# Performance work log

Hardware: AMD Instinct MI355X
Metric: run time of the kernel (lower is better)

## Reference

```python
import jax, jax.numpy as jnp
import numpy as np

N_NODES = 50000
N_EDGES = 800000
D_IN = 128
D_HID = 128
N_CLASSES = 10
N_GRAPHS = 64


def setup_inputs() -> dict:
    key = jax.random.key(0)
    ks = jax.random.split(key, 12)
    x = jax.random.normal(ks[0], (N_NODES, D_IN), dtype=jnp.float32)
    edge_index = jax.random.randint(ks[1], (2, N_EDGES), 0, N_NODES, dtype=jnp.int32)
    batch = jnp.sort(jax.random.randint(ks[2], (N_NODES,), 0, N_GRAPHS, dtype=jnp.int32))
    s = 0.05
    conv0_w = jax.random.normal(ks[3], (D_IN, D_HID), dtype=jnp.float32) * s
    conv0_b = jax.random.normal(ks[4], (D_HID,), dtype=jnp.float32) * s
    conv1_w = jax.random.normal(ks[5], (D_HID, D_HID), dtype=jnp.float32) * s
    conv1_b = jax.random.normal(ks[6], (D_HID,), dtype=jnp.float32) * s
    lin0_w = jax.random.normal(ks[7], (D_HID, D_HID), dtype=jnp.float32) * s
    lin0_b = jax.random.normal(ks[8], (D_HID,), dtype=jnp.float32) * s
    lin1_w = jax.random.normal(ks[9], (D_HID, N_CLASSES), dtype=jnp.float32) * s
    lin1_b = jax.random.normal(ks[10], (N_CLASSES,), dtype=jnp.float32) * s
    return dict(x=x, edge_index=edge_index, batch=batch,
                conv0_w=conv0_w, conv0_b=conv0_b,
                conv1_w=conv1_w, conv1_b=conv1_b,
                lin0_w=lin0_w, lin0_b=lin0_b,
                lin1_w=lin1_w, lin1_b=lin1_b)


def gcn_conv(x, edge_index, w, b):
    # PyG GCNConv: linear transform, add self-loops, D^-1/2 (A+I) D^-1/2 aggregation, + bias
    n = x.shape[0]
    h = x @ w  # [N, out]
    loop = jnp.arange(n, dtype=edge_index.dtype)
    row = jnp.concatenate([edge_index[0], loop])  # source nodes
    col = jnp.concatenate([edge_index[1], loop])  # destination nodes
    deg = jax.ops.segment_sum(jnp.ones_like(col, dtype=h.dtype), col, num_segments=n)
    dinv = jnp.where(deg > 0, jax.lax.rsqrt(deg), 0.0)
    norm = dinv[row] * dinv[col]  # [E+N]
    msg = h[row] * norm[:, None]  # gather + scale
    out = jax.ops.segment_sum(msg, col, num_segments=n)  # scatter-add
    return out + b


def reference(x, edge_index, batch, conv0_w, conv0_b, conv1_w, conv1_b,
              lin0_w, lin0_b, lin1_w, lin1_b):
    h = jax.nn.relu(gcn_conv(x, edge_index, conv0_w, conv0_b))
    h = jax.nn.relu(gcn_conv(h, edge_index, conv1_w, conv1_b))
    # global max pooling over nodes of each graph
    h = jax.ops.segment_max(h, batch, num_segments=N_GRAPHS)  # [G, D_HID]
    # NOTE: original applies relu after EVERY linear, including the output layer
    h = jax.nn.relu(h @ lin0_w + lin0_b)
    h = jax.nn.relu(h @ lin1_w + lin1_b)
    return jax.nn.log_softmax(h, axis=-1)
```

## Files before the change

kernel.cpp:

```cpp
#include <hip/hip_runtime.h>

#define D 128
#define BINCAP 6144
#define P2CAP 6144

typedef __attribute__((ext_vector_type(8))) short short8;
typedef __attribute__((ext_vector_type(4))) float f32x4;

__device__ inline unsigned short f2bf(float f) {
    unsigned u = __float_as_uint(f);
    return (unsigned short)((u + 0x7FFFu + ((u >> 16) & 1u)) >> 16);
}
__device__ inline float bflo(unsigned u) { return __uint_as_float(u << 16); }
__device__ inline float bfhi(unsigned u) { return __uint_as_float(u & 0xFFFF0000u); }

__global__ __launch_bounds__(256) void k_initW(const float* __restrict__ w0, const float* __restrict__ w1,
                                               const float* __restrict__ b0, const float* __restrict__ b1,
                                               uint4* __restrict__ Wp0, uint4* __restrict__ Wp1,
                                               float* __restrict__ b0p, float* __restrict__ b1p,
                                               int* __restrict__ binCur, int* __restrict__ pool, int nbins) {
    int t = threadIdx.x, b = blockIdx.x;
    int e = b * 256 + t;
    {
        int l = e & 63, U = (e >> 6) & 7, T = e >> 9;
        int nn = U * 16 + (l & 15);
        int kq = T * 32 + ((l >> 4) << 3);
        unsigned r[4], s[4];
#pragma unroll
        for (int jj = 0; jj < 4; ++jj) {
            int k0 = kq + 2 * jj, k1 = k0 + 1;
            unsigned a0 = f2bf(w0[k0 * 128 + nn]), a1 = f2bf(w0[k1 * 128 + nn]);
            r[jj] = a0 | (a1 << 16);
            int c0 = ((k0 & 7) << 4) | (k0 >> 3), c1 = ((k1 & 7) << 4) | (k1 >> 3);
            unsigned q0 = f2bf(w1[c0 * 128 + nn]), q1 = f2bf(w1[c1 * 128 + nn]);
            s[jj] = q0 | (q1 << 16);
        }
        Wp0[e] = make_uint4(r[0], r[1], r[2], r[3]);
        Wp1[e] = make_uint4(s[0], s[1], s[2], s[3]);
    }
    if (b == 0) {
        if (t < nbins) binCur[t] = t * BINCAP;
        for (int i = t; i < 64 * 128; i += 256) pool[i] = 0;
    }
    if (b == 1 && t < 128) {
        int c = ((t & 7) << 4) | (t >> 3);
        b0p[t] = b0[c];
        b1p[t] = b1[c];
    }
}

__global__ __launch_bounds__(256) void k_p1scatter(const int* __restrict__ row, const int* __restrict__ col,
                                                   int* __restrict__ binCur, unsigned* __restrict__ ebuf, int E) {
    __shared__ int h[256], s[256], delta[256], lcur[256];
    __shared__ unsigned stage[4096];
    int t = threadIdx.x;
    h[t] = 0;
    __syncthreads();
    int base = blockIdx.x * 4096;
    int cnt = min(4096, E - base);
    if (cnt == 4096) {
        int myc[16], myr[16];
        const int4* c4 = (const int4*)(col + base);
        const int4* r4 = (const int4*)(row + base);
#pragma unroll
        for (int k = 0; k < 4; ++k) {
            int4 cv = c4[t * 4 + k];
            int4 rv = r4[t * 4 + k];
            myc[k * 4 + 0] = cv.x; myc[k * 4 + 1] = cv.y; myc[k * 4 + 2] = cv.z; myc[k * 4 + 3] = cv.w;
            myr[k * 4 + 0] = rv.x; myr[k * 4 + 1] = rv.y; myr[k * 4 + 2] = rv.z; myr[k * 4 + 3] = rv.w;
        }
#pragma unroll
        for (int k = 0; k < 16; ++k) atomicAdd(&h[myc[k] >> 8], 1);
        __syncthreads();
        int v = h[t];
        s[t] = v;
        __syncthreads();
        for (int off = 1; off < 256; off <<= 1) {
            int tmp = (t >= off) ? s[t - off] : 0;
            __syncthreads();
            s[t] += tmp;
            __syncthreads();
        }
        int excl = s[t] - v;
        lcur[t] = excl;
        delta[t] = (v > 0) ? (atomicAdd(&binCur[t], v) - excl) : 0;
        __syncthreads();
#pragma unroll
        for (int k = 0; k < 16; ++k) {
            int d = myc[k];
            int slot = atomicAdd(&lcur[d >> 8], 1);
            stage[slot] = ((unsigned)d << 16) | (unsigned)myr[k];
        }
        __syncthreads();
#pragma unroll
        for (int k = 0; k < 16; ++k) {
            int slot = k * 256 + t;
            unsigned vv = stage[slot];
            int b = vv >> 24;
            ebuf[delta[b] + slot] = vv;
        }
    } else {
        for (int k = 0; k < 16; ++k) {
            int e = base + k * 256 + t;
            if (e < E) atomicAdd(&h[col[e] >> 8], 1);
        }
        __syncthreads();
        int v = h[t];
        s[t] = v;
        __syncthreads();
        for (int off = 1; off < 256; off <<= 1) {
            int tmp = (t >= off) ? s[t - off] : 0;
            __syncthreads();
            s[t] += tmp;
            __syncthreads();
        }
        int excl = s[t] - v;
        lcur[t] = excl;
        delta[t] = (v > 0) ? (atomicAdd(&binCur[t], v) - excl) : 0;
        __syncthreads();
        for (int k = 0; k < 16; ++k) {
            int e = base + k * 256 + t;
            if (e < E) {
                int d = col[e];
                int slot = atomicAdd(&lcur[d >> 8], 1);
                stage[slot] = ((unsigned)d << 16) | (unsigned)row[e];
            }
        }
        __syncthreads();
        for (int k = 0; k < 16; ++k) {
            int slot = k * 256 + t;
            if (slot < cnt) {
                unsigned vv = stage[slot];
                int b = vv >> 24;
                ebuf[delta[b] + slot] = vv;
            }
        }
    }
}

__global__ __launch_bounds__(256) void k_p2sort(const unsigned* __restrict__ ebuf, const int* __restrict__ binCur,
                                                int* __restrict__ csr, int* __restrict__ off_, int* __restrict__ end_,
                                                float* __restrict__ dinv, int n) {
    __shared__ unsigned stage[P2CAP];
    __shared__ unsigned stage2[P2CAP];
    __shared__ int h[256], s[256], cur[256];
    int b = blockIdx.x, t = threadIdx.x;
    int beg = b * BINCAP;
    int cnt = binCur[b] - beg;
    h[t] = 0;
    __syncthreads();
    int nfull = cnt >> 2;
    const uint4* e4 = (const uint4*)(ebuf + beg);
    uint4* st4 = (uint4*)stage;
    for (int i = t; i < nfull; i += 256) {
        uint4 v = e4[i];
        st4[i] = v;
        atomicAdd(&h[(v.x >> 16) & 0xFF], 1);
        atomicAdd(&h[(v.y >> 16) & 0xFF], 1);
        atomicAdd(&h[(v.z >> 16) & 0xFF], 1);
        atomicAdd(&h[(v.w >> 16) & 0xFF], 1);
    }
    for (int i = (nfull << 2) + t; i < cnt; i += 256) {
        unsigned v = ebuf[beg + i];
        stage[i] = v;
        atomicAdd(&h[(v >> 16) & 0xFF], 1);
    }
    __syncthreads();
    int v = h[t];
    s[t] = v;
    __syncthreads();
    for (int off = 1; off < 256; off <<= 1) {
        int tmp = (t >= off) ? s[t - off] : 0;
        __syncthreads();
        s[t] += tmp;
        __syncthreads();
    }
    int excl = s[t] - v;
    cur[t] = excl;
    int d = b * 256 + t;
    if (d < n) {
        off_[d] = beg + excl;
        end_[d] = beg + excl + v;
        dinv[d] = rsqrtf((float)(v + 1));
    }
    __syncthreads();
    for (int i = t; i < cnt; i += 256) {
        unsigned vv = stage[i];
        int slot = atomicAdd(&cur[(vv >> 16) & 0xFF], 1);
        stage2[slot] = vv & 0xFFFFu;
    }
    __syncthreads();
    uint4* c4o = (uint4*)(csr + beg);
    uint4* st24 = (uint4*)stage2;
    for (int i = t; i < nfull; i += 256) c4o[i] = st24[i];
    for (int i = (nfull << 2) + t; i < cnt; i += 256) csr[beg + i] = (int)stage2[i];
}

__global__ __launch_bounds__(256) void k_gemm0(const float* __restrict__ x, const uint4* __restrict__ Wp,
                                               const float* __restrict__ dinv, unsigned* __restrict__ outb, int n) {
    int wave = threadIdx.x >> 6, l = threadIdx.x & 63;
    int mt = blockIdx.x * 4 + wave;
    int r0 = mt * 16;
    if (r0 >= n) return;
    int rowA = r0 + (l & 15);
    int kq = (l >> 4) * 8;
    f32x4 acc[8];
#pragma unroll
    for (int U = 0; U < 8; ++U) acc[U] = (f32x4){0.f, 0.f, 0.f, 0.f};
    const float* xr = x + (size_t)rowA * 128 + kq;
#pragma unroll
    for (int T = 0; T < 4; ++T) {
        float4 a0 = *(const float4*)(xr + T * 32);
        float4 a1 = *(const float4*)(xr + T * 32 + 4);
        short8 af;
        af[0] = (short)f2bf(a0.x); af[1] = (short)f2bf(a0.y);
        af[2] = (short)f2bf(a0.z); af[3] = (short)f2bf(a0.w);
        af[4] = (short)f2bf(a1.x); af[5] = (short)f2bf(a1.y);
        af[6] = (short)f2bf(a1.z); af[7] = (short)f2bf(a1.w);
#pragma unroll
        for (int U = 0; U < 8; ++U) {
            short8 bf = *(const short8*)&Wp[(T * 8 + U) * 64 + l];
            acc[U] = __builtin_amdgcn_mfma_f32_16x16x32_bf16(af, bf, acc[U], 0, 0, 0);
        }
    }
    int rq = l >> 4, cl = l & 15;
#pragma unroll
    for (int q = 0; q < 4; ++q) {
        int rr = r0 + rq * 4 + q;
        float d = dinv[rr];
        uint4 w;
        w.x = (unsigned)f2bf(acc[0][q] * d) | ((unsigned)f2bf(acc[1][q] * d) << 16);
        w.y = (unsigned)f2bf(acc[2][q] * d) | ((unsigned)f2bf(acc[3][q] * d) << 16);
        w.z = (unsigned)f2bf(acc[4][q] * d) | ((unsigned)f2bf(acc[5][q] * d) << 16);
        w.w = (unsigned)f2bf(acc[6][q] * d) | ((unsigned)f2bf(acc[7][q] * d) << 16);
        *(uint4*)(outb + (size_t)rr * 64 + cl * 4) = w;
    }
}

__device__ inline void gather4(const uint4* __restrict__ hp4, const int* __restrict__ csr,
                               int q, int beg, int len, float acc[8]) {
    int maxlen = len;
    maxlen = max(maxlen, __shfl_xor(maxlen, 16, 64));
    maxlen = max(maxlen, __shfl_xor(maxlen, 32, 64));
    int j = 0;
    for (; j + 2 <= maxlen; j += 2) {
        bool a0 = (j < len), a1 = (j + 1 < len);
        int s0 = 0, s1 = 0;
        if (a0) s0 = csr[beg + j];
        if (a1) s1 = csr[beg + j + 1];
        uint4 u0, u1;
        if (a0) u0 = hp4[(size_t)s0 * 16 + q];
        if (a1) u1 = hp4[(size_t)s1 * 16 + q];
        if (a0) {
            acc[0] += bflo(u0.x); acc[1] += bfhi(u0.x);
            acc[2] += bflo(u0.y); acc[3] += bfhi(u0.y);
            acc[4] += bflo(u0.z); acc[5] += bfhi(u0.z);
            acc[6] += bflo(u0.w); acc[7] += bfhi(u0.w);
        }
        if (a1) {
            acc[0] += bflo(u1.x); acc[1] += bfhi(u1.x);
            acc[2] += bflo(u1.y); acc[3] += bfhi(u1.y);
            acc[4] += bflo(u1.z); acc[5] += bfhi(u1.z);
            acc[6] += bflo(u1.w); acc[7] += bfhi(u1.w);
        }
    }
    for (; j < maxlen; ++j) {
        if (j < len) {
            int s0 = csr[beg + j];
            uint4 u = hp4[(size_t)s0 * 16 + q];
            acc[0] += bflo(u.x); acc[1] += bfhi(u.x);
            acc[2] += bflo(u.y); acc[3] += bfhi(u.y);
            acc[4] += bflo(u.z); acc[5] += bfhi(u.z);
            acc[6] += bflo(u.w); acc[7] += bfhi(u.w);
        }
    }
}

__global__ __launch_bounds__(256) void k_aggemm(const unsigned* __restrict__ hp, const int* __restrict__ off_,
                                                const int* __restrict__ end_, const int* __restrict__ csr,
                                                const float* __restrict__ dinv, const float* __restrict__ bp,
                                                const uint4* __restrict__ Wp, unsigned* __restrict__ outb, int n) {
    __shared__ uint4 sA[16 * 17];
    int w = threadIdx.x >> 6, l = threadIdx.x & 63;
    int g = l >> 4, q = l & 15;
    int r0 = blockIdx.x * 16;
    int node = r0 + w * 4 + g;
    const uint4* hp4 = (const uint4*)hp;
    float acc[8];
    uint4 us = hp4[(size_t)node * 16 + q];
    acc[0] = bflo(us.x); acc[1] = bfhi(us.x);
    acc[2] = bflo(us.y); acc[3] = bfhi(us.y);
    acc[4] = bflo(us.z); acc[5] = bfhi(us.z);
    acc[6] = bflo(us.w); acc[7] = bfhi(us.w);
    int beg = off_[node];
    int len = end_[node] - beg;
    gather4(hp4, csr, q, beg, len, acc);
    float d0 = dinv[node];
    const float4* bp4 = (const float4*)bp;
    float4 ba = bp4[q * 2], bb = bp4[q * 2 + 1];
    uint4 pk;
    pk.x = (unsigned)f2bf(fmaxf(fmaf(d0, acc[0], ba.x), 0.f)) | ((unsigned)f2bf(fmaxf(fmaf(d0, acc[1], ba.y), 0.f)) << 16);
    pk.y = (unsigned)f2bf(fmaxf(fmaf(d0, acc[2], ba.z), 0.f)) | ((unsigned)f2bf(fmaxf(fmaf(d0, acc[3], ba.w), 0.f)) << 16);
    pk.z = (unsigned)f2bf(fmaxf(fmaf(d0, acc[4], bb.x), 0.f)) | ((unsigned)f2bf(fmaxf(fmaf(d0, acc[5], bb.y), 0.f)) << 16);
    pk.w = (unsigned)f2bf(fmaxf(fmaf(d0, acc[6], bb.z), 0.f)) | ((unsigned)f2bf(fmaxf(fmaf(d0, acc[7], bb.w), 0.f)) << 16);
    sA[(w * 4 + g) * 17 + q] = pk;
    __syncthreads();
    int rq = l >> 4, cl = l & 15;
    f32x4 c0v = (f32x4){0.f, 0.f, 0.f, 0.f}, c1v = (f32x4){0.f, 0.f, 0.f, 0.f};
#pragma unroll
    for (int T = 0; T < 4; ++T) {
        short8 af = *(const short8*)&sA[(l & 15) * 17 + T * 4 + rq];
        short8 bf0 = *(const short8*)&Wp[(T * 8 + 2 * w) * 64 + l];
        short8 bf1 = *(const short8*)&Wp[(T * 8 + 2 * w + 1) * 64 + l];
        c0v = __builtin_amdgcn_mfma_f32_16x16x32_bf16(af, bf0, c0v, 0, 0, 0);
        c1v = __builtin_amdgcn_mfma_f32_16x16x32_bf16(af, bf1, c1v, 0, 0, 0);
    }
#pragma unroll
    for (int qq = 0; qq < 4; ++qq) {
        int rr = r0 + rq * 4 + qq;
        float d2 = dinv[rr];
        unsigned pkk = (unsigned)f2bf(c0v[qq] * d2) | ((unsigned)f2bf(c1v[qq] * d2) << 16);
        outb[(size_t)rr * 64 + cl * 4 + w] = pkk;
    }
}

__global__ __launch_bounds__(256) void k_agg1(const unsigned* __restrict__ hp, const int* __restrict__ off_,
                                              const int* __restrict__ end_, const int* __restrict__ csr,
                                              const float* __restrict__ dinv, const float* __restrict__ bp,
                                              const int* __restrict__ batch, int* __restrict__ pool, int n) {
    __shared__ float2 sv[16][64];
    __shared__ int sg[16];
    int w = threadIdx.x >> 6, l = threadIdx.x & 63;
    int g = l >> 4, q = l & 15;
    int node = blockIdx.x * 16 + w * 4 + g;
    const uint4* hp4 = (const uint4*)hp;
    float acc[8];
    uint4 us = hp4[(size_t)node * 16 + q];
    acc[0] = bflo(us.x); acc[1] = bfhi(us.x);
    acc[2] = bflo(us.y); acc[3] = bfhi(us.y);
    acc[4] = bflo(us.z); acc[5] = bfhi(us.z);
    acc[6] = bflo(us.w); acc[7] = bfhi(us.w);
    int beg = off_[node];
    int len = end_[node] - beg;
    gather4(hp4, csr, q, beg, len, acc);
    float d0 = dinv[node];
    const float4* bp4 = (const float4*)bp;
    float4 ba = bp4[q * 2], bb = bp4[q * 2 + 1];
    int rowi = w * 4 + g;
    sv[rowi][q * 4 + 0] = make_float2(fmaxf(fmaf(d0, acc[0], ba.x), 0.f), fmaxf(fmaf(d0, acc[1], ba.y), 0.f));
    sv[rowi][q * 4 + 1] = make_float2(fmaxf(fmaf(d0, acc[2], ba.z), 0.f), fmaxf(fmaf(d0, acc[3], ba.w), 0.f));
    sv[rowi][q * 4 + 2] = make_float2(fmaxf(fmaf(d0, acc[4], bb.x), 0.f), fmaxf(fmaf(d0, acc[5], bb.y), 0.f));
    sv[rowi][q * 4 + 3] = make_float2(fmaxf(fmaf(d0, acc[6], bb.z), 0.f), fmaxf(fmaf(d0, acc[7], bb.w), 0.f));
    if (q == 0) sg[rowi] = batch[node];
    __syncthreads();
    if (threadIdx.x < 64) {
        int t = threadIdx.x;
        int c0 = 32 * (t & 3) + (t >> 2);
        int cur = sg[0];
        float2 m = sv[0][t];
        for (int ww = 1; ww < 16; ++ww) {
            int gg = sg[ww];
            float2 vv = sv[ww][t];
            if (gg == cur) { m.x = fmaxf(m.x, vv.x); m.y = fmaxf(m.y, vv.y); }
            else {
                atomicMax(&pool[cur * 128 + c0], __float_as_int(m.x));
                atomicMax(&pool[cur * 128 + c0 + 16], __float_as_int(m.y));
                cur = gg; m = vv;
            }
        }
        atomicMax(&pool[cur * 128 + c0], __float_as_int(m.x));
        atomicMax(&pool[cur * 128 + c0 + 16], __float_as_int(m.y));
    }
}

__global__ __launch_bounds__(128) void k_mlp(const float* __restrict__ pool, const float* __restrict__ W0,
                                             const float* __restrict__ b0, const float* __restrict__ W1,
                                             const float* __restrict__ b1, float* __restrict__ out) {
    __shared__ float rowv[128];
    __shared__ float h2[128];
    __shared__ float h3[10];
    int g = blockIdx.x, t = threadIdx.x;
    rowv[t] = pool[g * 128 + t];
    __syncthreads();
    float acc = b0[t];
    for (int k = 0; k < 128; ++k) acc = fmaf(rowv[k], W0[k * 128 + t], acc);
    h2[t] = fmaxf(acc, 0.f);
    __syncthreads();
    if (t < 10) {
        float a = b1[t];
        for (int k = 0; k < 128; ++k) a = fmaf(h2[k], W1[k * 10 + t], a);
        h3[t] = fmaxf(a, 0.f);
    }
    __syncthreads();
    if (t == 0) {
        float mx = h3[0];
        for (int j = 1; j < 10; ++j) mx = fmaxf(mx, h3[j]);
        float s = 0.f;
        for (int j = 0; j < 10; ++j) s += expf(h3[j] - mx);
        float lse = logf(s) + mx;
        for (int j = 0; j < 10; ++j) out[g * 10 + j] = h3[j] - lse;
    }
}

extern "C" void kernel_launch(void* const* d_in, const int* in_sizes, int n_in,
                              void* d_out, int out_size, void* d_ws, size_t ws_size,
                              hipStream_t stream) {
    const float* x   = (const float*)d_in[0];
    const int* eidx  = (const int*)d_in[1];
    const int* batch = (const int*)d_in[2];
    const float* w0  = (const float*)d_in[3];
    const float* b0  = (const float*)d_in[4];
    const float* w1  = (const float*)d_in[5];
    const float* b1  = (const float*)d_in[6];
    const float* lw0 = (const float*)d_in[7];
    const float* lb0 = (const float*)d_in[8];
    const float* lw1 = (const float*)d_in[9];
    const float* lb1 = (const float*)d_in[10];
    float* out = (float*)d_out;

    int n = in_sizes[2];
    int E = in_sizes[1] / 2;
    const int* row = eidx;
    const int* col = eidx + E;
    int nbins = (n + 255) >> 8;
    int nb1 = (E + 4095) / 4096;

    char* ws = (char*)d_ws;
    size_t o = 0;
    auto take = [&](size_t bytes) { void* p = ws + o; o += (bytes + 255) & ~(size_t)255; return p; };
    int*      binCur   = (int*)     take(256 * 4);
    int*      off_     = (int*)     take((size_t)n * 4);
    int*      end_     = (int*)     take((size_t)n * 4);
    float*    dinv     = (float*)   take((size_t)n * 4);
    int*      csr      = (int*)     take(((size_t)nbins * BINCAP + 64) * 4);
    unsigned* ebuf     = (unsigned*)take(((size_t)nbins * BINCAP + 64) * 4);
    uint4*    Wp0      = (uint4*)   take(2048 * 16);
    uint4*    Wp1      = (uint4*)   take(2048 * 16);
    float*    b0p      = (float*)   take(128 * 4);
    float*    b1p      = (float*)   take(128 * 4);
    unsigned* h0b      = (unsigned*)take((size_t)n * 64 * 4);
    unsigned* h1b      = (unsigned*)take((size_t)n * 64 * 4);
    int*      pool     = (int*)     take(64 * 128 * 4);

    k_initW<<<8, 256, 0, stream>>>(w0, w1, b0, b1, Wp0, Wp1, b0p, b1p, binCur, pool, nbins);
    k_p1scatter<<<nb1, 256, 0, stream>>>(row, col, binCur, ebuf, E);
    k_p2sort<<<nbins, 256, 0, stream>>>(ebuf, binCur, csr, off_, end_, dinv, n);

    int mtBlocks = ((n + 15) / 16 + 3) / 4;

    k_gemm0<<<mtBlocks, 256, 0, stream>>>(x, Wp0, dinv, h0b, n);
    k_aggemm<<<n / 16, 256, 0, stream>>>(h0b, off_, end_, csr, dinv, b0p, Wp1, h1b, n);
    k_agg1<<<n / 16, 256, 0, stream>>>(h1b, off_, end_, csr, dinv, b1p, batch, pool, n);
    k_mlp<<<64, 128, 0, stream>>>((const float*)pool, lw0, lb0, lw1, lb1, out);
}
```

Before: 209.2 us.

## Fuse weight-prep into edge scatter kernel and pool via wavefront shuffles

Merges the weight packing/init kernel into the edge binning kernel as extra blocks, with binCur now zeroed by a memset and bin offsets added on the fly. This removes one kernel launch and its serialization. The global max-pool in the last aggregation kernel now merges same-graph rows inside each wavefront with shuffles instead of going through shared memory and a block barrier. That cuts LDS traffic and a __syncthreads, but each wavefront now issues its own atomics, giving up to four times as many atomicMax calls per block.

```diff
diff --git a/kernel.cpp b/kernel.cpp
--- a/kernel.cpp
+++ b/kernel.cpp
@@ -14,49 +14,48 @@
 __device__ inline float bflo(unsigned u) { return __uint_as_float(u << 16); }
 __device__ inline float bfhi(unsigned u) { return __uint_as_float(u & 0xFFFF0000u); }
 
-__global__ __launch_bounds__(256) void k_initW(const float* __restrict__ w0, const float* __restrict__ w1,
-                                               const float* __restrict__ b0, const float* __restrict__ b1,
-                                               uint4* __restrict__ Wp0, uint4* __restrict__ Wp1,
-                                               float* __restrict__ b0p, float* __restrict__ b1p,
-                                               int* __restrict__ binCur, int* __restrict__ pool, int nbins) {
-    int t = threadIdx.x, b = blockIdx.x;
-    int e = b * 256 + t;
-    {
-        int l = e & 63, U = (e >> 6) & 7, T = e >> 9;
-        int nn = U * 16 + (l & 15);
-        int kq = T * 32 + ((l >> 4) << 3);
-        unsigned r[4], s[4];
-#pragma unroll
-        for (int jj = 0; jj < 4; ++jj) {
-            int k0 = kq + 2 * jj, k1 = k0 + 1;
-            unsigned a0 = f2bf(w0[k0 * 128 + nn]), a1 = f2bf(w0[k1 * 128 + nn]);
-            r[jj] = a0 | (a1 << 16);
-            int c0 = ((k0 & 7) << 4) | (k0 >> 3), c1 = ((k1 & 7) << 4) | (k1 >> 3);
-            unsigned q0 = f2bf(w1[c0 * 128 + nn]), q1 = f2bf(w1[c1 * 128 + nn]);
-            s[jj] = q0 | (q1 << 16);
-        }
-        Wp0[e] = make_uint4(r[0], r[1], r[2], r[3]);
-        Wp1[e] = make_uint4(s[0], s[1], s[2], s[3]);
-    }
-    if (b == 0) {
-        if (t < nbins) binCur[t] = t * BINCAP;
-        for (int i = t; i < 64 * 128; i += 256) pool[i] = 0;
-    }
-    if (b == 1 && t < 128) {
-        int c = ((t & 7) << 4) | (t >> 3);
-        b0p[t] = b0[c];
-        b1p[t] = b1[c];
-    }
-}
-
-__global__ __launch_bounds__(256) void k_p1scatter(const int* __restrict__ row, const int* __restrict__ col,
-                                                   int* __restrict__ binCur, unsigned* __restrict__ ebuf, int E) {
+__global__ __launch_bounds__(256) void k_prep(const int* __restrict__ row, const int* __restrict__ col, int E, int nb1,
+                                              const float* __restrict__ w0, const float* __restrict__ w1,
+                                              const float* __restrict__ b0, const float* __restrict__ b1,
+                                              uint4* __restrict__ Wp0, uint4* __restrict__ Wp1,
+                                              float* __restrict__ b0p, float* __restrict__ b1p,
+                                              int* __restrict__ binCur, unsigned* __restrict__ ebuf,
+                                              int* __restrict__ pool) {
+    int b = blockIdx.x, t = threadIdx.x;
+    if (b >= nb1) {
+        int bb = b - nb1;
+        if (bb < 8) {
+            int e = bb * 256 + t;
+            int l = e & 63, U = (e >> 6) & 7, T = e >> 9;
+            int nn = U * 16 + (l & 15);
+            int kq = T * 32 + ((l >> 4) << 3);
+            unsigned r[4], s[4];
+#pragma unroll
+            for (int jj = 0; jj < 4; ++jj) {
+                int k0 = kq + 2 * jj, k1 = k0 + 1;
+                unsigned a0 = f2bf(w0[k0 * 128 + nn]), a1 = f2bf(w0[k1 * 128 + nn]);
+                r[jj] = a0 | (a1 << 16);
+                int c0 = ((k0 & 7) << 4) | (k0 >> 3), c1 = ((k1 & 7) << 4) | (k1 >> 3);
+                unsigned q0 = f2bf(w1[c0 * 128 + nn]), q1 = f2bf(w1[c1 * 128 + nn]);
+                s[jj] = q0 | (q1 << 16);
+            }
+            Wp0[e] = make_uint4(r[0], r[1], r[2], r[3]);
+            Wp1[e] = make_uint4(s[0], s[1], s[2], s[3]);
+        } else {
+            for (int i = t; i < 64 * 128; i += 256) pool[i] = 0;
+            if (t < 128) {
+                int c = ((t & 7) << 4) | (t >> 3);
+                b0p[t] = b0[c];
+                b1p[t] = b1[c];
+            }
+        }
+        return;
+    }
     __shared__ int h[256], s[256], delta[256], lcur[256];
     __shared__ unsigned stage[4096];
-    int t = threadIdx.x;
     h[t] = 0;
     __syncthreads();
-    int base = blockIdx.x * 4096;
+    int base = b * 4096;
     int cnt = min(4096, E - base);
     if (cnt == 4096) {
         int myc[16], myr[16];
@@ -83,7 +82,7 @@
         }
         int excl = s[t] - v;
         lcur[t] = excl;
-        delta[t] = (v > 0) ? (atomicAdd(&binCur[t], v) - excl) : 0;
+        delta[t] = t * BINCAP + ((v > 0) ? atomicAdd(&binCur[t], v) : 0) - excl;
         __syncthreads();
 #pragma unroll
         for (int k = 0; k < 16; ++k) {
@@ -96,8 +95,7 @@
         for (int k = 0; k < 16; ++k) {
             int slot = k * 256 + t;
             unsigned vv = stage[slot];
-            int b = vv >> 24;
-            ebuf[delta[b] + slot] = vv;
+            ebuf[delta[vv >> 24] + slot] = vv;
         }
     } else {
         for (int k = 0; k < 16; ++k) {
@@ -116,7 +114,7 @@
         }
         int excl = s[t] - v;
         lcur[t] = excl;
-        delta[t] = (v > 0) ? (atomicAdd(&binCur[t], v) - excl) : 0;
+        delta[t] = t * BINCAP + ((v > 0) ? atomicAdd(&binCur[t], v) : 0) - excl;
         __syncthreads();
         for (int k = 0; k < 16; ++k) {
             int e = base + k * 256 + t;
@@ -131,8 +129,7 @@
             int slot = k * 256 + t;
             if (slot < cnt) {
                 unsigned vv = stage[slot];
-                int b = vv >> 24;
-                ebuf[delta[b] + slot] = vv;
+                ebuf[delta[vv >> 24] + slot] = vv;
             }
         }
     }
@@ -146,7 +143,7 @@
     __shared__ int h[256], s[256], cur[256];
     int b = blockIdx.x, t = threadIdx.x;
     int beg = b * BINCAP;
-    int cnt = binCur[b] - beg;
+    int cnt = binCur[b];
     h[t] = 0;
     __syncthreads();
     int nfull = cnt >> 2;
@@ -328,8 +325,6 @@
                                               const int* __restrict__ end_, const int* __restrict__ csr,
                                               const float* __restrict__ dinv, const float* __restrict__ bp,
                                               const int* __restrict__ batch, int* __restrict__ pool, int n) {
-    __shared__ float2 sv[16][64];
-    __shared__ int sg[16];
     int w = threadIdx.x >> 6, l = threadIdx.x & 63;
     int g = l >> 4, q = l & 15;
     int node = blockIdx.x * 16 + w * 4 + g;
@@ -346,30 +341,28 @@
     float d0 = dinv[node];
     const float4* bp4 = (const float4*)bp;
     float4 ba = bp4[q * 2], bb = bp4[q * 2 + 1];
-    int rowi = w * 4 + g;
-    sv[rowi][q * 4 + 0] = make_float2(fmaxf(fmaf(d0, acc[0], ba.x), 0.f), fmaxf(fmaf(d0, acc[1], ba.y), 0.f));
-    sv[rowi][q * 4 + 1] = make_float2(fmaxf(fmaf(d0, acc[2], ba.z), 0.f), fmaxf(fmaf(d0, acc[3], ba.w), 0.f));
-    sv[rowi][q * 4 + 2] = make_float2(fmaxf(fmaf(d0, acc[4], bb.x), 0.f), fmaxf(fmaf(d0, acc[5], bb.y), 0.f));
-    sv[rowi][q * 4 + 3] = make_float2(fmaxf(fmaf(d0, acc[6], bb.z), 0.f), fmaxf(fmaf(d0, acc[7], bb.w), 0.f));
-    if (q == 0) sg[rowi] = batch[node];
-    __syncthreads();
-    if (threadIdx.x < 64) {
-        int t = threadIdx.x;
-        int c0 = 32 * (t & 3) + (t >> 2);
-        int cur = sg[0];
-        float2 m = sv[0][t];
-        for (int ww = 1; ww < 16; ++ww) {
-            int gg = sg[ww];
-            float2 vv = sv[ww][t];
-            if (gg == cur) { m.x = fmaxf(m.x, vv.x); m.y = fmaxf(m.y, vv.y); }
-            else {
-                atomicMax(&pool[cur * 128 + c0], __float_as_int(m.x));
-                atomicMax(&pool[cur * 128 + c0 + 16], __float_as_int(m.y));
-                cur = gg; m = vv;
-            }
-        }
-        atomicMax(&pool[cur * 128 + c0], __float_as_int(m.x));
-        atomicMax(&pool[cur * 128 + c0 + 16], __float_as_int(m.y));
+    float v[8];
+    v[0] = fmaxf(fmaf(d0, acc[0], ba.x), 0.f); v[1] = fmaxf(fmaf(d0, acc[1], ba.y), 0.f);
+    v[2] = fmaxf(fmaf(d0, acc[2], ba.z), 0.f); v[3] = fmaxf(fmaf(d0, acc[3], ba.w), 0.f);
+    v[4] = fmaxf(fmaf(d0, acc[4], bb.x), 0.f); v[5] = fmaxf(fmaf(d0, acc[5], bb.y), 0.f);
+    v[6] = fmaxf(fmaf(d0, acc[6], bb.z), 0.f); v[7] = fmaxf(fmaf(d0, acc[7], bb.w), 0.f);
+    int bid = batch[node];
+#pragma unroll
+    for (int dshift = 16; dshift <= 32; dshift <<= 1) {
+        int pb = __shfl_up(bid, dshift, 64);
+        bool mrg = (l >= dshift) && (pb == bid);
+#pragma unroll
+        for (int k = 0; k < 8; ++k) {
+            float pv = __shfl_up(v[k], dshift, 64);
+            if (mrg) v[k] = fmaxf(v[k], pv);
+        }
+    }
+    int nb_ = __shfl_down(bid, 16, 64);
+    bool tail = (g == 3) || (nb_ != bid);
+    if (tail) {
+#pragma unroll
+        for (int k = 0; k < 8; ++k)
+            atomicMax(&pool[bid * 128 + k * 16 + q], __float_as_int(v[k]));
     }
 }
 
@@ -442,8 +435,9 @@
     unsigned* h1b      = (unsigned*)take((size_t)n * 64 * 4);
     int*      pool     = (int*)     take(64 * 128 * 4);
 
-    k_initW<<<8, 256, 0, stream>>>(w0, w1, b0, b1, Wp0, Wp1, b0p, b1p, binCur, pool, nbins);
-    k_p1scatter<<<nb1, 256, 0, stream>>>(row, col, binCur, ebuf, E);
+    hipMemsetAsync(binCur, 0, 256 * 4, stream);
+    k_prep<<<nb1 + 9, 256, 0, stream>>>(row, col, E, nb1, w0, w1, b0, b1,
+                                        Wp0, Wp1, b0p, b1p, binCur, ebuf, pool);
     k_p2sort<<<nbins, 256, 0, stream>>>(ebuf, binCur, csr, off_, end_, dinv, n);
 
     int mtBlocks = ((n + 15) / 16 + 3) / 4;
```

Result: no change. 211.2 us (+0.9%).
